# Optimization experiments

Hardware: AMD Instinct MI355X
Metric: run time of the kernel (lower is better)

The kernel has to match this reference:

```python
import jax, jax.numpy as jnp
import numpy as np

N_NODES = 100000
N_EDGES = 1600000
IN_DIM = 3
LATENT = 128
LATENT_DEC = 128
NUM_LAYER = 2      # shared-weight middle GCN layers
NUM_LAYER_DEC = 2  # shared-weight middle decoder layers


def _glorot(key, shape):
    fan_in, fan_out = shape[0], shape[1]
    lim = np.sqrt(6.0 / (fan_in + fan_out)).astype(np.float32)
    return jax.random.uniform(key, shape, jnp.float32, -lim, lim)


def setup_inputs() -> dict:
    key = jax.random.key(0)
    ks = jax.random.split(key, 10)
    x = jax.random.normal(ks[0], (N_NODES, IN_DIM), jnp.float32)
    edge_index = jax.random.randint(ks[1], (2, N_EDGES), 0, N_NODES, jnp.int64)
    return {
        "x": x,
        "edge_index": edge_index,
        "W_s": _glorot(ks[2], (IN_DIM, LATENT)),   "b_s": jnp.zeros((LATENT,), jnp.float32),
        "W_m": _glorot(ks[3], (LATENT, LATENT)),   "b_m": jnp.zeros((LATENT,), jnp.float32),
        "W_e": _glorot(ks[4], (LATENT, LATENT)),   "b_e": jnp.zeros((LATENT,), jnp.float32),
        "W_sd": _glorot(ks[5], (LATENT, LATENT_DEC)),    "b_sd": jnp.zeros((LATENT_DEC,), jnp.float32),
        "W_md": _glorot(ks[6], (LATENT_DEC, LATENT_DEC)),"b_md": jnp.zeros((LATENT_DEC,), jnp.float32),
        "W_ed": _glorot(ks[7], (LATENT_DEC, IN_DIM)),    "b_ed": jnp.zeros((IN_DIM,), jnp.float32),
    }


def _gcn_conv(h, W, b, src, dst, dinv):
    # PyG GCNConv: out_i = sum_j norm_ij * (x_j @ W) + b, norm = d^-1/2_i d^-1/2_j
    h = h @ W
    norm = dinv[src] * dinv[dst]                       # [E+N]
    msg = norm[:, None] * h[src]                       # gather + scale
    out = jax.ops.segment_sum(msg, dst, num_segments=N_NODES)  # scatter-add
    return out + b


def reference(x, edge_index, W_s, b_s, W_m, b_m, W_e, b_e, W_sd, b_sd, W_md, b_md, W_ed, b_ed):
    loops = jnp.arange(N_NODES, dtype=edge_index.dtype)
    src = jnp.concatenate([edge_index[0], loops])      # add self-loops
    dst = jnp.concatenate([edge_index[1], loops])
    deg = jax.ops.segment_sum(jnp.ones(src.shape[0], x.dtype), dst, num_segments=N_NODES)
    dinv = jnp.where(deg > 0, jax.lax.rsqrt(deg), 0.0)

    h = jax.nn.relu(_gcn_conv(x, W_s, b_s, src, dst, dinv))
    for _ in range(NUM_LAYER):  # shared weights (ModuleList([layer]*n))
        h = jax.nn.relu(_gcn_conv(h, W_m, b_m, src, dst, dinv))
    h = jax.nn.relu(_gcn_conv(h, W_e, b_e, src, dst, dinv))

    h = jax.nn.relu(h @ W_sd + b_sd)
    for _ in range(NUM_LAYER_DEC):  # shared weights
        h = jax.nn.relu(h @ W_md + b_md)
    y = h @ W_ed + b_ed
    return y + x
```

## Files before the change

kernel.cpp:

```cpp
#include <hip/hip_runtime.h>


typedef __attribute__((ext_vector_type(8))) short short8;
typedef __attribute__((ext_vector_type(4))) float floatx4;
typedef __attribute__((ext_vector_type(2))) float floatx2;

#define BIN_CH 8192
#define NBMAX 512
#define BKT 256
#define HS_STRIDE 68

__device__ __forceinline__ unsigned short f2bf(float f) {
    unsigned int u = __float_as_uint(f);
    u += 0x7fffu + ((u >> 16) & 1u);
    return (unsigned short)(u >> 16);
}
__device__ __forceinline__ unsigned int pk_bf(float a, float b) {
    return (unsigned int)f2bf(a) | ((unsigned int)f2bf(b) << 16);
}
__device__ __forceinline__ unsigned char f2fp8(float f) {
    return (unsigned char)(__builtin_amdgcn_cvt_pk_fp8_f32(f, f, 0, false) & 0xFF);
}
__device__ __forceinline__ short8 ld_frag(const unsigned short* p) {
    uint2 a = *(const uint2*)p;
    uint2 b = *(const uint2*)(p + 4);
    int4 v = make_int4((int)a.x, (int)a.y, (int)b.x, (int)b.y);
    return __builtin_bit_cast(short8, v);
}


__global__ void pack_kernel(const float* __restrict__ W0, const float* __restrict__ W1,
                            const float* __restrict__ W2, const float* __restrict__ W3,
                            unsigned short* __restrict__ P0, unsigned short* __restrict__ P1,
                            unsigned short* __restrict__ P2, unsigned short* __restrict__ P3,
                            int* __restrict__ gfill, unsigned char* __restrict__ t8zrowA,
                            unsigned char* __restrict__ t8zrowB, int NB) {
    if (blockIdx.x == 0) {
        for (int i = threadIdx.x; i < NB; i += 256) gfill[i] = 0;
        if (threadIdx.x < 32) {
            ((unsigned int*)t8zrowA)[threadIdx.x] = 0;
            ((unsigned int*)t8zrowB)[threadIdx.x] = 0;
        }
    }
    int which = blockIdx.x >> 3;
    const float* W = which == 0 ? W0 : which == 1 ? W1 : which == 2 ? W2 : W3;
    unsigned short* P = which == 0 ? P0 : which == 1 ? P1 : which == 2 ? P2 : P3;
    int f = (blockIdx.x & 7) * 256 + threadIdx.x;
    int lane = f & 63, nt = (f >> 6) & 7, kc = f >> 9;
    int kbase = kc * 32 + (lane >> 4) * 8;
    int ncol = nt * 16 + (lane & 15);
    short8 frag;
    #pragma unroll
    for (int j = 0; j < 8; ++j)
        frag[j] = (short)f2bf(W[(size_t)(kbase + j) * 128 + ncol]);
    *((short8*)(P + (size_t)f * 8)) = frag;
}


__global__ __launch_bounds__(512) void bin_kernel(
        const int* __restrict__ src, const int* __restrict__ dst,
        int* __restrict__ gfill, unsigned int* __restrict__ binbuf,
        int NB, int C, int E) {
    __shared__ int h4[4][NBMAX];
    __shared__ int start[NBMAX];
    __shared__ int tot[NBMAX];
    __shared__ int dstoff[NBMAX];
    int tid = threadIdx.x;
    int grp = tid >> 7;
    int e0 = blockIdx.x * BIN_CH;
    for (int i = tid; i < 4 * NBMAX; i += 512) ((int*)h4)[i] = 0;
    __syncthreads();
    for (int i = tid; i < BIN_CH; i += 512) {
        int e = e0 + i;
        if (e < E) atomicAdd(&h4[grp][dst[e] >> 8], 1);
    }
    __syncthreads();
    if (tid < 64) {
        int carry = 0;
        for (int base = 0; base < NB; base += 64) {
            int idx = base + tid;
            int c0 = 0, c1 = 0, c2 = 0, c3 = 0, v = 0;
            if (idx < NB) {
                c0 = h4[0][idx]; c1 = h4[1][idx];
                c2 = h4[2][idx]; c3 = h4[3][idx];
                v = c0 + c1 + c2 + c3;
            }
            int s = v;
            #pragma unroll
            for (int off = 1; off < 64; off <<= 1) {
                int u = __shfl_up(s, off);
                if (tid >= off) s += u;
            }
            if (idx < NB) {
                int ex = carry + s - v;
                start[idx] = ex;
                tot[idx] = v;
                h4[0][idx] = ex;
                h4[1][idx] = ex + c0;
                h4[2][idx] = ex + c0 + c1;
                h4[3][idx] = ex + c0 + c1 + c2;
            }
            carry += __shfl(s, 63);
        }
    }
    __syncthreads();
    for (int i = tid; i < NB; i += 512) {
        int cnt = tot[i];
        int g = cnt ? atomicAdd(&gfill[i], cnt) : 0;
        dstoff[i] = g - start[i];
    }
    __syncthreads();
    for (int i = tid; i < BIN_CH; i += 512) {
        int e = e0 + i;
        if (e >= E) continue;
        int d = dst[e];
        int b = d >> 8;
        int slot = atomicAdd(&h4[grp][b], 1);
        int gidx = b * C + dstoff[b] + slot;
        if (gidx < (b + 1) * C)
            binbuf[gidx] = (unsigned int)src[e] | ((unsigned int)(d & 255) << 17);
    }
}

__global__ __launch_bounds__(256) void build_kernel(
        const unsigned int* __restrict__ binbuf, const int* __restrict__ gfill,
        int* __restrict__ rowptr, float* __restrict__ dinv, int* __restrict__ col,
        int NB, int C, int N, int E) {
    __shared__ int h4[4][BKT];
    __shared__ int hs[BKT];
    __shared__ int tot[BKT];
    __shared__ int bbase_s;
    int b = blockIdx.x, tid = threadIdx.x;
    int grp = tid >> 6;
    int cnt = gfill[b];
    const unsigned int* p = binbuf + (size_t)b * C;
    for (int i = tid; i < 4 * BKT; i += 256) ((int*)h4)[i] = 0;
    __syncthreads();
    if (tid >= 64 && tid < 128) {
        int l = tid - 64;
        int s = 0;
        for (int i = l; i < b; i += 64) s += gfill[i];
        #pragma unroll
        for (int off = 32; off > 0; off >>= 1) s += __shfl_down(s, off);
        if (l == 0) bbase_s = s;
    }
    for (int i = tid; i < cnt; i += 256) atomicAdd(&h4[grp][p[i] >> 17], 1);
    __syncthreads();
    if (tid < 64) {
        int carry = 0;
        for (int base = 0; base < BKT; base += 64) {
            int idx = base + tid;
            int c0 = h4[0][idx], c1 = h4[1][idx], c2 = h4[2][idx], c3 = h4[3][idx];
            int v = c0 + c1 + c2 + c3;
            int s = v;
            #pragma unroll
            for (int off = 1; off < 64; off <<= 1) {
                int u = __shfl_up(s, off);
                if (tid >= off) s += u;
            }
            int ex = carry + s - v;
            hs[idx] = ex;
            tot[idx] = v;
            h4[0][idx] = ex;
            h4[1][idx] = ex + c0;
            h4[2][idx] = ex + c0 + c1;
            h4[3][idx] = ex + c0 + c1 + c2;
            carry += __shfl(s, 63);
        }
    }
    __syncthreads();
    int base = bbase_s;
    if (tid < BKT) {
        int node = b * BKT + tid;
        if (node < N) {
            rowptr[node] = base + hs[tid];
            dinv[node] = 1.0f / sqrtf((float)(tot[tid] + 1));
        }
    }
    if (b == 0 && tid == 0) rowptr[N] = E;
    __syncthreads();
    for (int i = tid; i < cnt; i += 256) {
        unsigned int u = p[i];
        int local = u >> 17;
        int pos = atomicAdd(&h4[grp][local], 1);
        col[base + pos] = (int)(u & 0x1FFFFu);
    }
}


__global__ void in_gemm_kernel(const float* __restrict__ x, const float* __restrict__ W,
                               const float* __restrict__ dinv,
                               unsigned char* __restrict__ t8, int n) {
    int g = blockIdx.x * 256 + threadIdx.x;
    int i = g >> 6, c2 = g & 63;
    if (i >= n) return;
    float x0 = x[i * 3], x1 = x[i * 3 + 1], x2 = x[i * 3 + 2];
    float d = dinv[i];
    int c = c2 * 2;
    float v0 = d * (x0 * W[c]     + x1 * W[128 + c]     + x2 * W[256 + c]);
    float v1 = d * (x0 * W[c + 1] + x1 * W[128 + c + 1] + x2 * W[256 + c + 1]);
    unsigned int pk = __builtin_amdgcn_cvt_pk_fp8_f32(v0, v1, 0, false);
    ((unsigned short*)t8)[(size_t)i * 64 + c2] = (unsigned short)(pk & 0xFFFF);
}


__device__ __forceinline__ void gemm_regs16(const short8 af[4], const unsigned short* Ws,
                                            int lane, floatx4 acc[8]) {
    #pragma unroll
    for (int nt = 0; nt < 8; ++nt) acc[nt] = (floatx4){0.f, 0.f, 0.f, 0.f};
    #pragma unroll
    for (int kc = 0; kc < 4; ++kc) {
        #pragma unroll
        for (int nt = 0; nt < 8; ++nt) {
            short8 bf = *((const short8*)(Ws + ((kc * 8 + nt) * 64 + lane) * 8));
            acc[nt] = __builtin_amdgcn_mfma_f32_16x16x32_bf16(af[kc], bf, acc[nt], 0, 0, 0);
        }
    }
}

__device__ __forceinline__ void gemm_lds16(const unsigned short* Hs, const unsigned short* Ws,
                                           int wav, int lane, floatx4 acc[8]) {
    int quad = lane >> 4, mrow = lane & 15;
    short8 af[4];
    #pragma unroll
    for (int kc = 0; kc < 4; ++kc)
        af[kc] = ld_frag(Hs + (wav * 16 + mrow) * HS_STRIDE + (kc * 4 + quad) * 8);
    gemm_regs16(af, Ws, lane, acc);
}

__device__ __forceinline__ void relu_store_hs16(
        unsigned short* Hs, const float* __restrict__ bias,
        floatx4 acc[8], int wav, int lane) {
    int quad = lane >> 4, mrow = lane & 15;
    #pragma unroll
    for (int nt = 0; nt < 8; ++nt) {
        int colc = nt * 16 + mrow;
        float bcol = bias[colc];
        #pragma unroll
        for (int r = 0; r < 4; ++r) {
            int rowl = wav * 16 + quad * 4 + r;
            Hs[rowl * HS_STRIDE + colc] = f2bf(fmaxf(acc[nt][r] + bcol, 0.f));
        }
    }
}


__device__ __forceinline__ void agg_to_hs(
        const unsigned char* __restrict__ t8, const int* __restrict__ rowptr,
        const int* __restrict__ col, const float* __restrict__ dinv,
        const float* __restrict__ bias, unsigned short* Hs, int n) {
    int tid = threadIdx.x;
    int lane = tid & 63;
    int q16 = lane >> 4;
    int lq  = lane & 15;
    int oct = (lane >> 3) & 1;
    int l8  = lane & 7;
    int qrow0 = (tid >> 4) * 4;
    const float4* b4 = (const float4*)bias;

    int nd0 = blockIdx.x * 128 + qrow0;
    int bg[4], dg[4];
    #pragma unroll
    for (int it = 0; it < 4; ++it) {
        int node = nd0 + it; if (node >= n) node = n - 1;
        bg[it] = rowptr[node];
        dg[it] = rowptr[node + 1] - bg[it];
    }
    int jv0 = (lq < dg[0])      ? col[bg[0] + lq]      : n;
    int jv1 = (lq + 16 < dg[0]) ? col[bg[0] + 16 + lq] : n;

    for (int it = 0; it < 4; ++it) {
        int rowl = qrow0 + it;
        int node = nd0 + it; if (node >= n) node = n - 1;
        floatx2 acc[8];
        #pragma unroll
        for (int i = 0; i < 8; ++i) acc[i] = (floatx2){0.f, 0.f};

        uint4 s = ((const uint4*)(t8 + (size_t)node * 128))[l8];

        int deg = dg[it];
        uint4 v[16];
        #pragma unroll
        for (int q = 0; q < 8; ++q) {
            int j = __shfl(jv0, q16 * 16 + q * 2 + oct);
            v[q] = ((const uint4*)(t8 + (size_t)j * 128))[l8];
        }
        #pragma unroll
        for (int q = 0; q < 8; ++q) {
            int j = __shfl(jv1, q16 * 16 + q * 2 + oct);
            v[8 + q] = ((const uint4*)(t8 + (size_t)j * 128))[l8];
        }
        int njv0 = n, njv1 = n;
        if (it < 3) {
            njv0 = (lq < dg[it + 1])      ? col[bg[it + 1] + lq]      : n;
            njv1 = (lq + 16 < dg[it + 1]) ? col[bg[it + 1] + 16 + lq] : n;
        }
        #pragma unroll
        for (int q = 0; q < 16; ++q) {
            acc[0] += __builtin_amdgcn_cvt_pk_f32_fp8(v[q].x, false);
            acc[1] += __builtin_amdgcn_cvt_pk_f32_fp8(v[q].x, true);
            acc[2] += __builtin_amdgcn_cvt_pk_f32_fp8(v[q].y, false);
            acc[3] += __builtin_amdgcn_cvt_pk_f32_fp8(v[q].y, true);
            acc[4] += __builtin_amdgcn_cvt_pk_f32_fp8(v[q].z, false);
            acc[5] += __builtin_amdgcn_cvt_pk_f32_fp8(v[q].z, true);
            acc[6] += __builtin_amdgcn_cvt_pk_f32_fp8(v[q].w, false);
            acc[7] += __builtin_amdgcn_cvt_pk_f32_fp8(v[q].w, true);
        }
        for (int base = 32; base < deg; base += 32) {
            int m = deg - base;
            int a0 = (lq < m)      ? col[bg[it] + base + lq]      : n;
            int a1 = (lq + 16 < m) ? col[bg[it] + base + 16 + lq] : n;
            #pragma unroll
            for (int q = 0; q < 8; ++q) {
                int j = __shfl(a0, q16 * 16 + q * 2 + oct);
                v[q] = ((const uint4*)(t8 + (size_t)j * 128))[l8];
            }
            #pragma unroll
            for (int q = 0; q < 8; ++q) {
                int j = __shfl(a1, q16 * 16 + q * 2 + oct);
                v[8 + q] = ((const uint4*)(t8 + (size_t)j * 128))[l8];
            }
            #pragma unroll
            for (int q = 0; q < 16; ++q) {
                acc[0] += __builtin_amdgcn_cvt_pk_f32_fp8(v[q].x, false);
                acc[1] += __builtin_amdgcn_cvt_pk_f32_fp8(v[q].x, true);
                acc[2] += __builtin_amdgcn_cvt_pk_f32_fp8(v[q].y, false);
                acc[3] += __builtin_amdgcn_cvt_pk_f32_fp8(v[q].y, true);
                acc[4] += __builtin_amdgcn_cvt_pk_f32_fp8(v[q].z, false);
                acc[5] += __builtin_amdgcn_cvt_pk_f32_fp8(v[q].z, true);
                acc[6] += __builtin_amdgcn_cvt_pk_f32_fp8(v[q].w, false);
                acc[7] += __builtin_amdgcn_cvt_pk_f32_fp8(v[q].w, true);
            }
        }
        #pragma unroll
        for (int i = 0; i < 8; ++i) {
            acc[i].x += __shfl_xor(acc[i].x, 8);
            acc[i].y += __shfl_xor(acc[i].y, 8);
        }
        acc[0] += __builtin_amdgcn_cvt_pk_f32_fp8(s.x, false);
        acc[1] += __builtin_amdgcn_cvt_pk_f32_fp8(s.x, true);
        acc[2] += __builtin_amdgcn_cvt_pk_f32_fp8(s.y, false);
        acc[3] += __builtin_amdgcn_cvt_pk_f32_fp8(s.y, true);
        acc[4] += __builtin_amdgcn_cvt_pk_f32_fp8(s.z, false);
        acc[5] += __builtin_amdgcn_cvt_pk_f32_fp8(s.z, true);
        acc[6] += __builtin_amdgcn_cvt_pk_f32_fp8(s.w, false);
        acc[7] += __builtin_amdgcn_cvt_pk_f32_fp8(s.w, true);

        float di = dinv[node];
        float o[16];
        #pragma unroll
        for (int k = 0; k < 4; ++k) {
            float4 bb = b4[l8 * 4 + k];
            o[k*4+0] = fmaxf(di * acc[k*2].x   + bb.x, 0.f);
            o[k*4+1] = fmaxf(di * acc[k*2].y   + bb.y, 0.f);
            o[k*4+2] = fmaxf(di * acc[k*2+1].x + bb.z, 0.f);
            o[k*4+3] = fmaxf(di * acc[k*2+1].y + bb.w, 0.f);
        }
        if (oct == 0) {
            unsigned short* hp = Hs + rowl * HS_STRIDE + l8 * 16;
            uint2 w;
            w.x = pk_bf(o[0],  o[1]);  w.y = pk_bf(o[2],  o[3]);
            *(uint2*)(hp)      = w;
            w.x = pk_bf(o[4],  o[5]);  w.y = pk_bf(o[6],  o[7]);
            *(uint2*)(hp + 4)  = w;
            w.x = pk_bf(o[8],  o[9]);  w.y = pk_bf(o[10], o[11]);
            *(uint2*)(hp + 8)  = w;
            w.x = pk_bf(o[12], o[13]); w.y = pk_bf(o[14], o[15]);
            *(uint2*)(hp + 12) = w;
        }
        jv0 = njv0; jv1 = njv1;
    }
}


__global__ __launch_bounds__(512, 4) void agg_gemm_kernel(
        const unsigned char* __restrict__ t8, const int* __restrict__ rowptr,
        const int* __restrict__ col, const float* __restrict__ dinv,
        const float* __restrict__ bias, const unsigned short* __restrict__ Wp,
        unsigned char* __restrict__ outp, int n) {
    __shared__ unsigned short Hs[128 * HS_STRIDE];
    agg_to_hs(t8, rowptr, col, dinv, bias, Hs, n);

    int tid = threadIdx.x;
    int wav = tid >> 6, lane = tid & 63;
    int quad = lane >> 4, mrow = lane & 15;
    int row0 = blockIdx.x * 128 + wav * 16;

    floatx4 acc[8];
    gemm_lds16(Hs, Wp, wav, lane, acc);

    int rbase = row0 + quad * 4;
    float dv[4];
    #pragma unroll
    for (int r = 0; r < 4; ++r)
        dv[r] = (rbase + r < n) ? dinv[rbase + r] : 0.f;
    #pragma unroll
    for (int nt = 0; nt < 8; ++nt) {
        int colc = nt * 16 + mrow;
        #pragma unroll
        for (int r = 0; r < 4; ++r) {
            int row = rbase + r;
            if (row < n)
                outp[(size_t)row * 128 + colc] = f2fp8(acc[nt][r] * dv[r]);
        }
    }
}


__global__ __launch_bounds__(512, 4) void agg_dec_kernel(
        const unsigned char* __restrict__ t8, const int* __restrict__ rowptr,
        const int* __restrict__ col, const float* __restrict__ dinv,
        const float* __restrict__ bias,
        const unsigned short* __restrict__ Wp_sd, const float* __restrict__ b_sd,
        const unsigned short* __restrict__ Wp_md, const float* __restrict__ b_md,
        const float* __restrict__ W_ed, const float* __restrict__ b_ed,
        const float* __restrict__ x, float* __restrict__ out, int n) {
    __shared__ unsigned short Hs[128 * HS_STRIDE];
    agg_to_hs(t8, rowptr, col, dinv, bias, Hs, n);

    int tid = threadIdx.x;
    int wav = tid >> 6, lane = tid & 63;
    int quad = lane >> 4, mrow = lane & 15;
    int row0 = blockIdx.x * 128 + wav * 16;

    floatx4 acc[8];
    gemm_lds16(Hs, Wp_sd, wav, lane, acc);
    relu_store_hs16(Hs, b_sd, acc, wav, lane);
    gemm_lds16(Hs, Wp_md, wav, lane, acc);
    relu_store_hs16(Hs, b_md, acc, wav, lane);
    gemm_lds16(Hs, Wp_md, wav, lane, acc);

    float wed[8][3];
    #pragma unroll
    for (int nt = 0; nt < 8; ++nt) {
        int c = nt * 16 + mrow;
        #pragma unroll
        for (int k = 0; k < 3; ++k) wed[nt][k] = W_ed[c * 3 + k];
    }
    #pragma unroll
    for (int r = 0; r < 4; ++r) {
        float s0 = 0.f, s1 = 0.f, s2 = 0.f;
        #pragma unroll
        for (int nt = 0; nt < 8; ++nt) {
            float v = fmaxf(acc[nt][r] + b_md[nt * 16 + mrow], 0.f);
            s0 += v * wed[nt][0]; s1 += v * wed[nt][1]; s2 += v * wed[nt][2];
        }
        #pragma unroll
        for (int off = 1; off < 16; off <<= 1) {
            s0 += __shfl_xor(s0, off);
            s1 += __shfl_xor(s1, off);
            s2 += __shfl_xor(s2, off);
        }
        if (mrow == 0) {
            int row = row0 + quad * 4 + r;
            if (row < n) {
                out[row * 3 + 0] = s0 + b_ed[0] + x[row * 3 + 0];
                out[row * 3 + 1] = s1 + b_ed[1] + x[row * 3 + 1];
                out[row * 3 + 2] = s2 + b_ed[2] + x[row * 3 + 2];
            }
        }
    }
}


extern "C" void kernel_launch(void* const* d_in, const int* in_sizes, int n_in,
                              void* d_out, int out_size, void* d_ws, size_t ws_size,
                              hipStream_t stream) {
    const float* x    = (const float*)d_in[0];
    const int*   ei   = (const int*)d_in[1];
    const float* W_s  = (const float*)d_in[2];
    const float* b_s  = (const float*)d_in[3];
    const float* W_m  = (const float*)d_in[4];
    const float* b_m  = (const float*)d_in[5];
    const float* W_e  = (const float*)d_in[6];
    const float* b_e  = (const float*)d_in[7];
    const float* W_sd = (const float*)d_in[8];
    const float* b_sd = (const float*)d_in[9];
    const float* W_md = (const float*)d_in[10];
    const float* b_md = (const float*)d_in[11];
    const float* W_ed = (const float*)d_in[12];
    const float* b_ed = (const float*)d_in[13];
    float* outp = (float*)d_out;

    const int N = in_sizes[0] / 3;
    const int E = in_sizes[1] / 2;
    const int* src = ei;
    const int* dst = ei + E;

    const int NB = (N + BKT - 1) / BKT;
    const int C  = (((E / NB) * 3 / 2) + 255) & ~255;

    char* p = (char*)d_ws;
    auto carve = [&](size_t bytes) {
        void* r = (void*)p;
        p += (bytes + 255) & ~(size_t)255;
        return r;
    };
    int*   rowptr = (int*)  carve((size_t)(N + 1) * 4);
    int*   col    = (int*)  carve((size_t)E * 4);
    float* dinv   = (float*)carve((size_t)N * 4);
    int*   gfill  = (int*)  carve((size_t)NB * 4);
    unsigned int* binbuf = (unsigned int*)carve((size_t)NB * C * 4);
    unsigned short* Wp_m  = (unsigned short*)carve(16384 * 2);
    unsigned short* Wp_e  = (unsigned short*)carve(16384 * 2);
    unsigned short* Wp_sd = (unsigned short*)carve(16384 * 2);
    unsigned short* Wp_md = (unsigned short*)carve(16384 * 2);
    unsigned char*  T8a = (unsigned char*) carve((size_t)(N + 1) * 128);
    unsigned char*  T8b = (unsigned char*) carve((size_t)(N + 1) * 128);
    (void)ws_size;

    const int gBin = (E + BIN_CH - 1) / BIN_CH;
    const int gRow128 = (N + 127) / 128;

    pack_kernel<<<32, 256, 0, stream>>>(W_m, W_e, W_sd, W_md, Wp_m, Wp_e, Wp_sd, Wp_md,
                                        gfill, T8a + (size_t)N * 128,
                                        T8b + (size_t)N * 128, NB);

    bin_kernel<<<gBin, 512, 0, stream>>>(src, dst, gfill, binbuf, NB, C, E);
    build_kernel<<<NB, 256, 0, stream>>>(binbuf, gfill, rowptr, dinv, col, NB, C, N, E);

    in_gemm_kernel<<<(N * 64 + 255) / 256, 256, 0, stream>>>(x, W_s, dinv, T8a, N);
    agg_gemm_kernel<<<gRow128, 512, 0, stream>>>(T8a, rowptr, col, dinv, b_s, Wp_m, T8b, N);
    agg_gemm_kernel<<<gRow128, 512, 0, stream>>>(T8b, rowptr, col, dinv, b_m, Wp_m, T8a, N);
    agg_gemm_kernel<<<gRow128, 512, 0, stream>>>(T8a, rowptr, col, dinv, b_m, Wp_e, T8b, N);

    agg_dec_kernel<<<gRow128, 512, 0, stream>>>(T8b, rowptr, col, dinv, b_e,
                                                Wp_sd, b_sd, Wp_md, b_md,
                                                W_ed, b_ed, x, outp, N);
}
```

Before: 392.4 us.

## Shrink aggregation blocks to 64 rows and drop software-pipelined neighbor prefetch

Aggregation kernels now use 256-thread blocks covering 64 rows instead of 512 threads over 128 rows, doubling the grid. The unrolled first-chunk gather and the prefetch of the next row's column indices are removed in favour of a simple per-row loop, and the self-feature load is moved after the neighbor loop. An explicit __syncthreads is added before the LDS GEMM. The intent is lower register pressure and finer-grained scheduling, at the cost of losing the overlap between index loads and gathers.

```diff
diff --git a/kernel.cpp b/kernel.cpp
--- a/kernel.cpp
+++ b/kernel.cpp
@@ -9,6 +9,7 @@
 #define NBMAX 512
 #define BKT 256
 #define HS_STRIDE 68
+#define ROWS 64
 
 __device__ __forceinline__ unsigned short f2bf(float f) {
     unsigned int u = __float_as_uint(f);
@@ -258,66 +259,29 @@
     int qrow0 = (tid >> 4) * 4;
     const float4* b4 = (const float4*)bias;
 
-    int nd0 = blockIdx.x * 128 + qrow0;
-    int bg[4], dg[4];
-    #pragma unroll
-    for (int it = 0; it < 4; ++it) {
-        int node = nd0 + it; if (node >= n) node = n - 1;
-        bg[it] = rowptr[node];
-        dg[it] = rowptr[node + 1] - bg[it];
-    }
-    int jv0 = (lq < dg[0])      ? col[bg[0] + lq]      : n;
-    int jv1 = (lq + 16 < dg[0]) ? col[bg[0] + 16 + lq] : n;
-
     for (int it = 0; it < 4; ++it) {
         int rowl = qrow0 + it;
-        int node = nd0 + it; if (node >= n) node = n - 1;
+        int node = blockIdx.x * ROWS + rowl;
+        if (node >= n) node = n - 1;
         floatx2 acc[8];
         #pragma unroll
         for (int i = 0; i < 8; ++i) acc[i] = (floatx2){0.f, 0.f};
 
-        uint4 s = ((const uint4*)(t8 + (size_t)node * 128))[l8];
-
-        int deg = dg[it];
-        uint4 v[16];
-        #pragma unroll
-        for (int q = 0; q < 8; ++q) {
-            int j = __shfl(jv0, q16 * 16 + q * 2 + oct);
-            v[q] = ((const uint4*)(t8 + (size_t)j * 128))[l8];
-        }
-        #pragma unroll
-        for (int q = 0; q < 8; ++q) {
-            int j = __shfl(jv1, q16 * 16 + q * 2 + oct);
-            v[8 + q] = ((const uint4*)(t8 + (size_t)j * 128))[l8];
-        }
-        int njv0 = n, njv1 = n;
-        if (it < 3) {
-            njv0 = (lq < dg[it + 1])      ? col[bg[it + 1] + lq]      : n;
-            njv1 = (lq + 16 < dg[it + 1]) ? col[bg[it + 1] + 16 + lq] : n;
-        }
-        #pragma unroll
-        for (int q = 0; q < 16; ++q) {
-            acc[0] += __builtin_amdgcn_cvt_pk_f32_fp8(v[q].x, false);
-            acc[1] += __builtin_amdgcn_cvt_pk_f32_fp8(v[q].x, true);
-            acc[2] += __builtin_amdgcn_cvt_pk_f32_fp8(v[q].y, false);
-            acc[3] += __builtin_amdgcn_cvt_pk_f32_fp8(v[q].y, true);
-            acc[4] += __builtin_amdgcn_cvt_pk_f32_fp8(v[q].z, false);
-            acc[5] += __builtin_amdgcn_cvt_pk_f32_fp8(v[q].z, true);
-            acc[6] += __builtin_amdgcn_cvt_pk_f32_fp8(v[q].w, false);
-            acc[7] += __builtin_amdgcn_cvt_pk_f32_fp8(v[q].w, true);
-        }
-        for (int base = 32; base < deg; base += 32) {
+        int beg = rowptr[node];
+        int deg = rowptr[node + 1] - beg;
+        for (int base = 0; base < deg; base += 32) {
             int m = deg - base;
-            int a0 = (lq < m)      ? col[bg[it] + base + lq]      : n;
-            int a1 = (lq + 16 < m) ? col[bg[it] + base + 16 + lq] : n;
+            int jv0 = (lq < m)      ? col[beg + base + lq]      : n;
+            int jv1 = (lq + 16 < m) ? col[beg + base + 16 + lq] : n;
+            uint4 v[16];
             #pragma unroll
             for (int q = 0; q < 8; ++q) {
-                int j = __shfl(a0, q16 * 16 + q * 2 + oct);
+                int j = __shfl(jv0, q16 * 16 + q * 2 + oct);
                 v[q] = ((const uint4*)(t8 + (size_t)j * 128))[l8];
             }
             #pragma unroll
             for (int q = 0; q < 8; ++q) {
-                int j = __shfl(a1, q16 * 16 + q * 2 + oct);
+                int j = __shfl(jv1, q16 * 16 + q * 2 + oct);
                 v[8 + q] = ((const uint4*)(t8 + (size_t)j * 128))[l8];
             }
             #pragma unroll
@@ -337,6 +301,7 @@
             acc[i].x += __shfl_xor(acc[i].x, 8);
             acc[i].y += __shfl_xor(acc[i].y, 8);
         }
+        uint4 s = ((const uint4*)(t8 + (size_t)node * 128))[l8];
         acc[0] += __builtin_amdgcn_cvt_pk_f32_fp8(s.x, false);
         acc[1] += __builtin_amdgcn_cvt_pk_f32_fp8(s.x, true);
         acc[2] += __builtin_amdgcn_cvt_pk_f32_fp8(s.y, false);
@@ -368,23 +333,23 @@
             w.x = pk_bf(o[12], o[13]); w.y = pk_bf(o[14], o[15]);
             *(uint2*)(hp + 12) = w;
         }
-        jv0 = njv0; jv1 = njv1;
-    }
-}
-
-
-__global__ __launch_bounds__(512, 4) void agg_gemm_kernel(
+    }
+}
+
+
+__global__ __launch_bounds__(256, 4) void agg_gemm_kernel(
         const unsigned char* __restrict__ t8, const int* __restrict__ rowptr,
         const int* __restrict__ col, const float* __restrict__ dinv,
         const float* __restrict__ bias, const unsigned short* __restrict__ Wp,
         unsigned char* __restrict__ outp, int n) {
-    __shared__ unsigned short Hs[128 * HS_STRIDE];
+    __shared__ unsigned short Hs[ROWS * HS_STRIDE];
     agg_to_hs(t8, rowptr, col, dinv, bias, Hs, n);
+    __syncthreads();
 
     int tid = threadIdx.x;
     int wav = tid >> 6, lane = tid & 63;
     int quad = lane >> 4, mrow = lane & 15;
-    int row0 = blockIdx.x * 128 + wav * 16;
+    int row0 = blockIdx.x * ROWS + wav * 16;
 
     floatx4 acc[8];
     gemm_lds16(Hs, Wp, wav, lane, acc);
@@ -407,7 +372,7 @@
 }
 
 
-__global__ __launch_bounds__(512, 4) void agg_dec_kernel(
+__global__ __launch_bounds__(256, 4) void agg_dec_kernel(
         const unsigned char* __restrict__ t8, const int* __restrict__ rowptr,
         const int* __restrict__ col, const float* __restrict__ dinv,
         const float* __restrict__ bias,
@@ -415,13 +380,14 @@
         const unsigned short* __restrict__ Wp_md, const float* __restrict__ b_md,
         const float* __restrict__ W_ed, const float* __restrict__ b_ed,
         const float* __restrict__ x, float* __restrict__ out, int n) {
-    __shared__ unsigned short Hs[128 * HS_STRIDE];
+    __shared__ unsigned short Hs[ROWS * HS_STRIDE];
     agg_to_hs(t8, rowptr, col, dinv, bias, Hs, n);
+    __syncthreads();
 
     int tid = threadIdx.x;
     int wav = tid >> 6, lane = tid & 63;
     int quad = lane >> 4, mrow = lane & 15;
-    int row0 = blockIdx.x * 128 + wav * 16;
+    int row0 = blockIdx.x * ROWS + wav * 16;
 
     floatx4 acc[8];
     gemm_lds16(Hs, Wp_sd, wav, lane, acc);
@@ -510,7 +476,7 @@
     (void)ws_size;
 
     const int gBin = (E + BIN_CH - 1) / BIN_CH;
-    const int gRow128 = (N + 127) / 128;
+    const int gRow64 = (N + ROWS - 1) / ROWS;
 
     pack_kernel<<<32, 256, 0, stream>>>(W_m, W_e, W_sd, W_md, Wp_m, Wp_e, Wp_sd, Wp_md,
                                         gfill, T8a + (size_t)N * 128,
@@ -520,11 +486,11 @@
     build_kernel<<<NB, 256, 0, stream>>>(binbuf, gfill, rowptr, dinv, col, NB, C, N, E);
 
     in_gemm_kernel<<<(N * 64 + 255) / 256, 256, 0, stream>>>(x, W_s, dinv, T8a, N);
-    agg_gemm_kernel<<<gRow128, 512, 0, stream>>>(T8a, rowptr, col, dinv, b_s, Wp_m, T8b, N);
-    agg_gemm_kernel<<<gRow128, 512, 0, stream>>>(T8b, rowptr, col, dinv, b_m, Wp_m, T8a, N);
-    agg_gemm_kernel<<<gRow128, 512, 0, stream>>>(T8a, rowptr, col, dinv, b_m, Wp_e, T8b, N);
-
-    agg_dec_kernel<<<gRow128, 512, 0, stream>>>(T8b, rowptr, col, dinv, b_e,
-                                                Wp_sd, b_sd, Wp_md, b_md,
-                                                W_ed, b_ed, x, outp, N);
-}
+    agg_gemm_kernel<<<gRow64, 256, 0, stream>>>(T8a, rowptr, col, dinv, b_s, Wp_m, T8b, N);
+    agg_gemm_kernel<<<gRow64, 256, 0, stream>>>(T8b, rowptr, col, dinv, b_m, Wp_m, T8a, N);
+    agg_gemm_kernel<<<gRow64, 256, 0, stream>>>(T8a, rowptr, col, dinv, b_m, Wp_e, T8b, N);
+
+    agg_dec_kernel<<<gRow64, 256, 0, stream>>>(T8b, rowptr, col, dinv, b_e,
+                                               Wp_sd, b_sd, Wp_md, b_md,
+                                               W_ed, b_ed, x, outp, N);
+}
```

After: 386.0 us. Within noise of the previous version (-1.6%).
